# Optimization experiments

Hardware: AMD Instinct MI355X
Metric: run time of the kernel (lower is better)

## Reference

```python
import jax, jax.numpy as jnp
import numpy as np

E = 1024  # embedding_dim
H = 64    # head_size

def setup_inputs() -> dict:
    key = jax.random.key(0)
    k1, k2, k3, k4 = jax.random.split(key, 4)
    x = jax.random.normal(k1, (4, 4096, E), dtype=jnp.float32)
    # nn.Linear(E, H, bias=False) weights have shape [H, E]; y = x @ W.T
    s = 1.0 / np.sqrt(E)
    Wq = jax.random.normal(k2, (H, E), dtype=jnp.float32) * s
    Wk = jax.random.normal(k3, (H, E), dtype=jnp.float32) * s
    Wv = jax.random.normal(k4, (H, E), dtype=jnp.float32) * s
    return {"x": x, "Wq": Wq, "Wk": Wk, "Wv": Wv}

def reference(x, Wq, Wk, Wv):
    B, T, E_ = x.shape
    q = jnp.einsum('bte,he->bth', x, Wq)
    k = jnp.einsum('bte,he->bth', x, Wk)
    v = jnp.einsum('bte,he->bth', x, Wv)
    # NOTE: original scales by sqrt(embedding_dim), not head_size
    scores = jnp.einsum('bqh,bkh->bqk', q, k) / jnp.sqrt(jnp.asarray(E_, x.dtype))
    causal = jnp.tril(jnp.ones((T, T), dtype=bool))
    scores = jnp.where(causal, scores, -jnp.inf)
    weights = jax.nn.softmax(scores, axis=-1)
    return jnp.einsum('bqk,bkh->bqh', weights, v)
```

## Files before the change

kernel.cpp:

```cpp
#include <hip/hip_runtime.h>
#include <stdint.h>

typedef __bf16 bf16x8 __attribute__((ext_vector_type(8)));
typedef float  f32x4  __attribute__((ext_vector_type(4)));

#define E_DIM 1024
#define H_DIM 64
#define T_SEQ 4096
#define B_BAT 4
#define M_TOT (B_BAT * T_SEQ)

__device__ __forceinline__ ushort f2bfu(float f) {
    return __builtin_bit_cast(ushort, (__bf16)f);
}
__device__ __forceinline__ uint32_t pk2(float lo, float hi) {
    return (uint32_t)f2bfu(lo) | ((uint32_t)f2bfu(hi) << 16);
}
__device__ __forceinline__ float ex2(float x) {
    return __builtin_amdgcn_exp2f(x);
}
__device__ __forceinline__ bf16x8 ldfrag(const ushort* p) {
    return __builtin_bit_cast(bf16x8, *(const uint4*)(p));
}
__device__ __forceinline__ void barrier_lgkm() {
    __builtin_amdgcn_s_waitcnt(0xC07F);
    __builtin_amdgcn_s_barrier();
}

__global__ __launch_bounds__(256) void wcvt(const float* __restrict__ Wq,
                                            const float* __restrict__ Wk,
                                            const float* __restrict__ Wv,
                                            ushort* __restrict__ Wfm) {
    int g = blockIdx.x * 256 + threadIdx.x;
    int n = g >> 7;
    int k8 = g & 127;
    const float* src = (n < 64) ? (Wq + (size_t)n * E_DIM)
                     : (n < 128) ? (Wk + (size_t)(n - 64) * E_DIM)
                     : (Wv + (size_t)(n - 128) * E_DIM);
    float sc = (n < 64) ? 0.045084220f : 1.0f;
    float4 a = *(const float4*)(src + k8 * 8);
    float4 b = *(const float4*)(src + k8 * 8 + 4);
    uint4 o;
    o.x = pk2(a.x * sc, a.y * sc); o.y = pk2(a.z * sc, a.w * sc);
    o.z = pk2(b.x * sc, b.y * sc); o.w = pk2(b.z * sc, b.w * sc);
    int s = k8 >> 3, kc = (k8 >> 2) & 1, qd = k8 & 3;
    int nt = n >> 4, lm = n & 15;
    int lane = qd * 16 + lm;
    *(uint4*)(Wfm + (((size_t)(s * 12 + nt) * 2 + kc) * 64 + lane) * 8) = o;
}

__global__ __launch_bounds__(256, 3) void qkv(const float* __restrict__ x,
                                              const ushort* __restrict__ Wfm,
                                              ushort* __restrict__ Qfm,
                                              ushort* __restrict__ Kfm,
                                              ushort* __restrict__ Vfm) {
    __shared__ union {
        ushort a[2][32 * 72];
        struct { ushort c[32 * 136]; ushort vt[64 * 40]; } epi;
    } sm;
    const int tid = threadIdx.x;
    const int w = tid >> 6, l = tid & 63;
    const int lm = l & 15, qd = l >> 4;
    const int m0 = blockIdx.x * 32;

    f32x4 acc[2][3];
#pragma unroll
    for (int r2 = 0; r2 < 2; ++r2)
#pragma unroll
        for (int t = 0; t < 3; ++t) acc[r2][t] = (f32x4){0.f, 0.f, 0.f, 0.f};

    const int srow = tid >> 3, kseg = tid & 7;
    const float* xsrc = x + (size_t)(m0 + srow) * E_DIM + kseg * 8;

    {
        float4 a0 = *(const float4*)xsrc;
        float4 a1 = *(const float4*)(xsrc + 4);
        uint4 u = {pk2(a0.x, a0.y), pk2(a0.z, a0.w), pk2(a1.x, a1.y), pk2(a1.z, a1.w)};
        *(uint4*)(&sm.a[0][srow * 72 + kseg * 8]) = u;
    }
    float4 xa0 = *(const float4*)(xsrc + 64);
    float4 xa1 = *(const float4*)(xsrc + 68);
    float4 xb0 = *(const float4*)(xsrc + 128);
    float4 xb1 = *(const float4*)(xsrc + 132);
    __syncthreads();

    for (int s = 0; s < 16; ++s) {
        const int cb = s & 1, nb = cb ^ 1;
        float4 xc0 = xa0, xc1 = xa1;
        if (s < 13) {
            xc0 = *(const float4*)(xsrc + (s + 3) * 64);
            xc1 = *(const float4*)(xsrc + (s + 3) * 64 + 4);
        }
        bf16x8 wf[3][2];
#pragma unroll
        for (int t = 0; t < 3; ++t)
#pragma unroll
            for (int kc = 0; kc < 2; ++kc)
                wf[t][kc] = ldfrag(Wfm + (((size_t)(s * 12 + w * 3 + t) * 2 + kc) * 64 + l) * 8);
        bf16x8 af[2][2];
#pragma unroll
        for (int r2 = 0; r2 < 2; ++r2)
#pragma unroll
            for (int kc = 0; kc < 2; ++kc)
                af[r2][kc] = ldfrag(&sm.a[cb][(r2 * 16 + lm) * 72 + kc * 32 + qd * 8]);
#pragma unroll
        for (int t = 0; t < 3; ++t)
#pragma unroll
            for (int kc = 0; kc < 2; ++kc)
#pragma unroll
                for (int r2 = 0; r2 < 2; ++r2)
                    acc[r2][t] = __builtin_amdgcn_mfma_f32_16x16x32_bf16(af[r2][kc], wf[t][kc], acc[r2][t], 0, 0, 0);
        if (s < 15) {
            uint4 u = {pk2(xa0.x, xa0.y), pk2(xa0.z, xa0.w), pk2(xa1.x, xa1.y), pk2(xa1.z, xa1.w)};
            *(uint4*)(&sm.a[nb][srow * 72 + kseg * 8]) = u;
        }
        xa0 = xb0; xa1 = xb1; xb0 = xc0; xb1 = xc1;
        if (s < 15) barrier_lgkm();
    }
    __syncthreads();

#pragma unroll
    for (int r2 = 0; r2 < 2; ++r2)
#pragma unroll
        for (int t = 0; t < 3; ++t) {
            int gc = w * 48 + t * 16 + lm;
            int m = r2 * 16 + qd * 4;
#pragma unroll
            for (int rr = 0; rr < 4; ++rr) {
                ushort v = f2bfu(acc[r2][t][rr]);
                if (gc < 128) sm.epi.c[(m + rr) * 136 + gc] = v;
                else          sm.epi.vt[(gc - 128) * 40 + (m + rr)] = v;
            }
        }
    __syncthreads();

    const int g16b = m0 >> 4;
    const int kt64 = m0 >> 6;
    const int tb   = (m0 >> 4) & 3;
    const int kcv  = (m0 >> 5) & 1;
#pragma unroll
    for (int ii = 0; ii < 3; ++ii) {
        int i = w + ii * 4;
        uint4 val;
        ushort* dst;
        if (i < 4) {
            int qt_l = i >> 1, kc = i & 1;
            val = *(const uint4*)(&sm.epi.c[(qt_l * 16 + lm) * 136 + kc * 32 + qd * 8]);
            dst = Qfm + (((size_t)(g16b + qt_l) * 2 + kc) * 64 + l) * 8;
        } else if (i < 8) {
            int j2 = i - 4, t_l = j2 >> 1, kc = j2 & 1;
            val = *(const uint4*)(&sm.epi.c[(t_l * 16 + lm) * 136 + 64 + kc * 32 + qd * 8]);
            dst = Kfm + (((size_t)((kt64 * 4 + tb + t_l) * 2 + kc)) * 64 + l) * 8;
        } else {
            int t = i - 8;
            val = *(const uint4*)(&sm.epi.vt[(t * 16 + lm) * 40 + qd * 8]);
            dst = Vfm + (((size_t)((kt64 * 4 + t) * 2 + kcv)) * 64 + l) * 8;
        }
        *(uint4*)dst = val;
    }
}

__global__ __launch_bounds__(256, 2) void flashm(const ushort* __restrict__ Qfm,
                                                 const ushort* __restrict__ Kfm,
                                                 const ushort* __restrict__ Vfm,
                                                 float* __restrict__ out) {
    __shared__ union {
        ushort plds[4][2][16 * 72];
        struct { float ro[4][16][68]; float rl[4][16]; } red;
    } sm;
    const int tid = threadIdx.x;
    const int wv = tid >> 6, l = tid & 63;
    const int lm = l & 15, qd = l >> 4;
    const int pr = blockIdx.x;
    const int bt = blockIdx.y;
    const int jA = pr, jB = 255 - pr;
    const int ktdA = jA >> 2, tdA = jA & 3;
    const int ktdB = jB >> 2, tdB = jB & 3;
    ushort* mypA = sm.plds[wv][0];
    ushort* mypB = sm.plds[wv][1];

    const ushort* kbase = Kfm + ((size_t)(bt * 64) * 8) * 512;
    const ushort* vbase = Vfm + ((size_t)(bt * 64) * 8) * 512;

    bf16x8 qA0, qA1, qB0, qB1;
    {
        const ushort* qp = Qfm + ((size_t)(bt * 256 + jA) * 2) * 512 + l * 8;
        qA0 = ldfrag(qp); qA1 = ldfrag(qp + 512);
        const ushort* qq = Qfm + ((size_t)(bt * 256 + jB) * 2) * 512 + l * 8;
        qB0 = ldfrag(qq); qB1 = ldfrag(qq + 512);
    }
    f32x4 oA[4], oB[4];
#pragma unroll
    for (int t = 0; t < 4; ++t) {
        oA[t] = (f32x4){0.f, 0.f, 0.f, 0.f};
        oB[t] = (f32x4){0.f, 0.f, 0.f, 0.f};
    }
    f32x4 lA = (f32x4){0.f, 0.f, 0.f, 0.f};
    f32x4 lB = (f32x4){0.f, 0.f, 0.f, 0.f};
    const bf16x8 ones = __builtin_bit_cast(bf16x8,
        (uint4){0x3F803F80u, 0x3F803F80u, 0x3F803F80u, 0x3F803F80u});

    auto emitP = [&](const f32x4* sf, ushort* wp, bool diag, int td) {
#pragma unroll
        for (int t = 0; t < 4; ++t) {
            if (!diag || t < td) {
                float p0 = ex2(sf[t][0]), p1 = ex2(sf[t][1]);
                float p2 = ex2(sf[t][2]), p3 = ex2(sf[t][3]);
                *(uint2*)(wp + t * 16) = uint2{pk2(p0, p1), pk2(p2, p3)};
            } else if (t == td) {
                float p[4];
#pragma unroll
                for (int rr = 0; rr < 4; ++rr) {
                    float pe = ex2(sf[t][rr]);
                    if (qd * 4 + rr > lm) pe = 0.f;
                    p[rr] = pe;
                }
                *(uint2*)(wp + t * 16) = uint2{pk2(p[0], p[1]), pk2(p[2], p[3])};
            } else {
                *(uint2*)(wp + t * 16) = uint2{0u, 0u};
            }
        }
    };
    auto pv = [&](const ushort* myp, const uint4 (&vu)[4][2], f32x4* o, f32x4& lac) {
        bf16x8 p0 = ldfrag(myp + lm * 72 + qd * 8);
        bf16x8 p1 = ldfrag(myp + lm * 72 + 32 + qd * 8);
#pragma unroll
        for (int t = 0; t < 4; ++t) {
            bf16x8 v0 = __builtin_bit_cast(bf16x8, vu[t][0]);
            bf16x8 v1 = __builtin_bit_cast(bf16x8, vu[t][1]);
            o[t] = __builtin_amdgcn_mfma_f32_16x16x32_bf16(p0, v0, o[t], 0, 0, 0);
            o[t] = __builtin_amdgcn_mfma_f32_16x16x32_bf16(p1, v1, o[t], 0, 0, 0);
        }
        lac = __builtin_amdgcn_mfma_f32_16x16x32_bf16(p0, ones, lac, 0, 0, 0);
        lac = __builtin_amdgcn_mfma_f32_16x16x32_bf16(p1, ones, lac, 0, 0, 0);
    };

    uint4 ku[8];
    {
        const ushort* kb = kbase + (size_t)wv * 8 * 512;
#pragma unroll
        for (int i = 0; i < 8; ++i) ku[i] = *(const uint4*)(kb + i * 512 + l * 8);
    }

#pragma unroll 1
    for (int kt = wv; kt <= ktdB; kt += 4) {
        const bool actA = (kt <= ktdA);
        const ushort* vb = vbase + (size_t)kt * 8 * 512;
        uint4 vu[4][2];
#pragma unroll
        for (int t = 0; t < 4; ++t) {
            vu[t][0] = *(const uint4*)(vb + (t * 2 + 0) * 512 + l * 8);
            vu[t][1] = *(const uint4*)(vb + (t * 2 + 1) * 512 + l * 8);
        }
        f32x4 sfA[4], sfB[4];
#pragma unroll
        for (int t = 0; t < 4; ++t) {
            sfA[t] = (f32x4){0.f, 0.f, 0.f, 0.f};
            sfB[t] = (f32x4){0.f, 0.f, 0.f, 0.f};
        }
#pragma unroll
        for (int t = 0; t < 4; ++t) {
            bf16x8 k0 = __builtin_bit_cast(bf16x8, ku[t * 2 + 0]);
            bf16x8 k1 = __builtin_bit_cast(bf16x8, ku[t * 2 + 1]);
            sfB[t] = __builtin_amdgcn_mfma_f32_16x16x32_bf16(k0, qB0, sfB[t], 0, 0, 0);
            sfB[t] = __builtin_amdgcn_mfma_f32_16x16x32_bf16(k1, qB1, sfB[t], 0, 0, 0);
            if (actA) {
                sfA[t] = __builtin_amdgcn_mfma_f32_16x16x32_bf16(k0, qA0, sfA[t], 0, 0, 0);
                sfA[t] = __builtin_amdgcn_mfma_f32_16x16x32_bf16(k1, qA1, sfA[t], 0, 0, 0);
            }
        }
        if (kt + 4 <= ktdB) {
            const ushort* kb = kbase + (size_t)(kt + 4) * 8 * 512;
#pragma unroll
            for (int i = 0; i < 8; ++i) ku[i] = *(const uint4*)(kb + i * 512 + l * 8);
        }
        emitP(sfB, mypB + lm * 72 + qd * 4, kt == ktdB, tdB);
        if (actA) emitP(sfA, mypA + lm * 72 + qd * 4, kt == ktdA, tdA);
        __builtin_amdgcn_wave_barrier();
        __builtin_amdgcn_s_waitcnt(0xC07F);
        __builtin_amdgcn_wave_barrier();
        pv(mypB, vu, oB, lB);
        if (actA) pv(mypA, vu, oA, lA);
        __builtin_amdgcn_wave_barrier();
    }

    __syncthreads();
    if (lm == 0) {
#pragma unroll
        for (int rr = 0; rr < 4; ++rr) sm.red.rl[wv][qd * 4 + rr] = lA[rr];
    }
#pragma unroll
    for (int t = 0; t < 4; ++t)
#pragma unroll
        for (int rr = 0; rr < 4; ++rr)
            sm.red.ro[wv][qd * 4 + rr][t * 16 + lm] = oA[t][rr];
    __syncthreads();
    {
        const int row = wv * 4 + qd;
        float ls = sm.red.rl[0][row] + sm.red.rl[1][row] + sm.red.rl[2][row] + sm.red.rl[3][row];
        float inv = 1.0f / ls;
        float4 s0 = *(const float4*)&sm.red.ro[0][row][lm * 4];
        float4 s1 = *(const float4*)&sm.red.ro[1][row][lm * 4];
        float4 s2 = *(const float4*)&sm.red.ro[2][row][lm * 4];
        float4 s3 = *(const float4*)&sm.red.ro[3][row][lm * 4];
        float4 ov;
        ov.x = (s0.x + s1.x + s2.x + s3.x) * inv;
        ov.y = (s0.y + s1.y + s2.y + s3.y) * inv;
        ov.z = (s0.z + s1.z + s2.z + s3.z) * inv;
        ov.w = (s0.w + s1.w + s2.w + s3.w) * inv;
        *(float4*)(out + ((size_t)bt * T_SEQ + jA * 16 + row) * 64 + lm * 4) = ov;
    }
    __syncthreads();
    if (lm == 0) {
#pragma unroll
        for (int rr = 0; rr < 4; ++rr) sm.red.rl[wv][qd * 4 + rr] = lB[rr];
    }
#pragma unroll
    for (int t = 0; t < 4; ++t)
#pragma unroll
        for (int rr = 0; rr < 4; ++rr)
            sm.red.ro[wv][qd * 4 + rr][t * 16 + lm] = oB[t][rr];
    __syncthreads();
    {
        const int row = wv * 4 + qd;
        float ls = sm.red.rl[0][row] + sm.red.rl[1][row] + sm.red.rl[2][row] + sm.red.rl[3][row];
        float inv = 1.0f / ls;
        float4 s0 = *(const float4*)&sm.red.ro[0][row][lm * 4];
        float4 s1 = *(const float4*)&sm.red.ro[1][row][lm * 4];
        float4 s2 = *(const float4*)&sm.red.ro[2][row][lm * 4];
        float4 s3 = *(const float4*)&sm.red.ro[3][row][lm * 4];
        float4 ov;
        ov.x = (s0.x + s1.x + s2.x + s3.x) * inv;
        ov.y = (s0.y + s1.y + s2.y + s3.y) * inv;
        ov.z = (s0.z + s1.z + s2.z + s3.z) * inv;
        ov.w = (s0.w + s1.w + s2.w + s3.w) * inv;
        *(float4*)(out + ((size_t)bt * T_SEQ + jB * 16 + row) * 64 + lm * 4) = ov;
    }
}

extern "C" void kernel_launch(void* const* d_in, const int* in_sizes, int n_in,
                              void* d_out, int out_size, void* d_ws, size_t ws_size,
                              hipStream_t stream) {
    const float* x  = (const float*)d_in[0];
    const float* Wq = (const float*)d_in[1];
    const float* Wk = (const float*)d_in[2];
    const float* Wv = (const float*)d_in[3];
    float* out = (float*)d_out;

    char* ws = (char*)d_ws;
    ushort* Wfm = (ushort*)(ws);
    ushort* Qfm = (ushort*)(ws + 393216);
    ushort* Kfm = (ushort*)(ws + 2490368);
    ushort* Vfm = (ushort*)(ws + 4587520);

    wcvt<<<96, 256, 0, stream>>>(Wq, Wk, Wv, Wfm);
    qkv<<<512, 256, 0, stream>>>(x, Wfm, Qfm, Kfm, Vfm);
    flashm<<<dim3(128, B_BAT), 256, 0, stream>>>(Qfm, Kfm, Vfm, out);
}
```

Baseline: 131.6 us.

## Prefetch W fragments one step ahead and shorten x register prefetch depth in QKV GEMM

```diff
diff --git a/kernel.cpp b/kernel.cpp
--- a/kernel.cpp
+++ b/kernel.cpp
@@ -49,7 +49,7 @@
     *(uint4*)(Wfm + (((size_t)(s * 12 + nt) * 2 + kc) * 64 + lane) * 8) = o;
 }
 
-__global__ __launch_bounds__(256, 3) void qkv(const float* __restrict__ x,
+__global__ __launch_bounds__(256, 2) void qkv(const float* __restrict__ x,
                                               const ushort* __restrict__ Wfm,
                                               ushort* __restrict__ Qfm,
                                               ushort* __restrict__ Kfm,
@@ -78,25 +78,31 @@
         uint4 u = {pk2(a0.x, a0.y), pk2(a0.z, a0.w), pk2(a1.x, a1.y), pk2(a1.z, a1.w)};
         *(uint4*)(&sm.a[0][srow * 72 + kseg * 8]) = u;
     }
-    float4 xa0 = *(const float4*)(xsrc + 64);
-    float4 xa1 = *(const float4*)(xsrc + 68);
-    float4 xb0 = *(const float4*)(xsrc + 128);
-    float4 xb1 = *(const float4*)(xsrc + 132);
+    float4 xn0 = *(const float4*)(xsrc + 64);
+    float4 xn1 = *(const float4*)(xsrc + 68);
+    bf16x8 wf[3][2];
+#pragma unroll
+    for (int t = 0; t < 3; ++t)
+#pragma unroll
+        for (int kc = 0; kc < 2; ++kc)
+            wf[t][kc] = ldfrag(Wfm + (((size_t)(0 * 12 + w * 3 + t) * 2 + kc) * 64 + l) * 8);
     __syncthreads();
 
     for (int s = 0; s < 16; ++s) {
         const int cb = s & 1, nb = cb ^ 1;
-        float4 xc0 = xa0, xc1 = xa1;
-        if (s < 13) {
-            xc0 = *(const float4*)(xsrc + (s + 3) * 64);
-            xc1 = *(const float4*)(xsrc + (s + 3) * 64 + 4);
-        }
-        bf16x8 wf[3][2];
-#pragma unroll
-        for (int t = 0; t < 3; ++t)
-#pragma unroll
-            for (int kc = 0; kc < 2; ++kc)
-                wf[t][kc] = ldfrag(Wfm + (((size_t)(s * 12 + w * 3 + t) * 2 + kc) * 64 + l) * 8);
+        float4 x20 = xn0, x21 = xn1;
+        if (s < 14) {
+            x20 = *(const float4*)(xsrc + (s + 2) * 64);
+            x21 = *(const float4*)(xsrc + (s + 2) * 64 + 4);
+        }
+        bf16x8 wfn[3][2];
+        if (s < 15) {
+#pragma unroll
+            for (int t = 0; t < 3; ++t)
+#pragma unroll
+                for (int kc = 0; kc < 2; ++kc)
+                    wfn[t][kc] = ldfrag(Wfm + (((size_t)((s + 1) * 12 + w * 3 + t) * 2 + kc) * 64 + l) * 8);
+        }
         bf16x8 af[2][2];
 #pragma unroll
         for (int r2 = 0; r2 < 2; ++r2)
@@ -111,10 +117,15 @@
                 for (int r2 = 0; r2 < 2; ++r2)
                     acc[r2][t] = __builtin_amdgcn_mfma_f32_16x16x32_bf16(af[r2][kc], wf[t][kc], acc[r2][t], 0, 0, 0);
         if (s < 15) {
-            uint4 u = {pk2(xa0.x, xa0.y), pk2(xa0.z, xa0.w), pk2(xa1.x, xa1.y), pk2(xa1.z, xa1.w)};
+            uint4 u = {pk2(xn0.x, xn0.y), pk2(xn0.z, xn0.w), pk2(xn1.x, xn1.y), pk2(xn1.z, xn1.w)};
             *(uint4*)(&sm.a[nb][srow * 72 + kseg * 8]) = u;
-        }
-        xa0 = xb0; xa1 = xb1; xb0 = xc0; xb1 = xc1;
+#pragma unroll
+            for (int t = 0; t < 3; ++t)
+#pragma unroll
+                for (int kc = 0; kc < 2; ++kc)
+                    wf[t][kc] = wfn[t][kc];
+        }
+        xn0 = x20; xn1 = x21;
         if (s < 15) barrier_lgkm();
     }
     __syncthreads();
```

Result: no change. 132.4 us (+0.6%).
